# Kernel tuning notes

Hardware: AMD Instinct MI355X
Metric: run time of the kernel (lower is better)

The kernel has to match this reference:

```python
import jax, jax.numpy as jnp
import numpy as np

N_NODES = 50000
NFEAT, NHID, NSSF, NCLASS = 512, 512, 256, 64
N_EDGES = 1600000
SP_RATE = 0.5
EPS = 1e-6


def spmm(src, dst, vals, m):
    # sparse [N,N] @ dense [N,F]: gather rows by src, scale, scatter-add to dst rows
    return jax.ops.segment_sum(m[src] * vals[:, None], dst, num_segments=N_NODES)


def setup_inputs() -> dict:
    key = jax.random.key(0)
    ks = jax.random.split(key, 12)
    stdv1 = 1.0 / np.sqrt(NFEAT)
    stdv2 = 1.0 / np.sqrt(NHID)
    inp = {
        "x": jax.random.normal(ks[0], (N_NODES, NFEAT), jnp.float32),
        "src": jax.random.randint(ks[1], (N_EDGES,), 0, N_NODES, jnp.int32),
        "dst": jax.random.randint(ks[2], (N_EDGES,), 0, N_NODES, jnp.int32),
        "vals": jax.random.uniform(ks[3], (N_EDGES,), jnp.float32),
        "W1": jax.random.uniform(ks[4], (NFEAT, NHID), jnp.float32, -stdv1, stdv1),
        "b1": jax.random.uniform(ks[5], (NHID,), jnp.float32, -stdv1, stdv1),
        "W2": jax.random.uniform(ks[6], (NHID, NHID), jnp.float32, -stdv2, stdv2),
        "b2": jax.random.uniform(ks[7], (NHID,), jnp.float32, -stdv2, stdv2),
        "W3": jax.random.uniform(ks[8], (NHID, NSSF), jnp.float32, -stdv2, stdv2),
        "b3": jax.random.uniform(ks[9], (NSSF,), jnp.float32, -stdv2, stdv2),
        "ssf": jax.random.normal(ks[10], (NSSF, NCLASS), jnp.float32) * 0.1,
        "sigma": jax.random.normal(ks[11], (), jnp.float32),
    }
    return inp


def reference(x, src, dst, vals, W1, b1, W2, b2, W3, b3, ssf, sigma):
    # 3 GCN layers: spmm(adj, x @ W + b)
    h = spmm(src, dst, vals, x @ W1 + b1)
    h = jax.nn.relu(h)
    h = spmm(src, dst, vals, h @ W2 + b2)
    h = jax.nn.relu(h)
    h = spmm(src, dst, vals, h @ W3 + b3)  # [N, NSSF]

    # sparsify subspace filter by magnitude threshold (static index)
    flat = jnp.abs(ssf).reshape(-1)
    filter_idx = round(NSSF * NCLASS * SP_RATE)
    threshold = jnp.sort(flat)[filter_idx]
    ssf_sp = jnp.where(jnp.abs(ssf) >= threshold, ssf, 0.0)

    out = h @ ssf_sp  # [N, NCLASS]

    # negative euclidean distance to each filter column: cdist(h, ssf_sp.T)
    sq = (jnp.sum(h * h, axis=1)[:, None]
          - 2.0 * out
          + jnp.sum(ssf_sp * ssf_sp, axis=0)[None, :])
    spatial_dist = -jnp.sqrt(jnp.maximum(sq, 1e-12))

    # cosine similarity of each row of h with each filter column
    hn = jnp.maximum(jnp.linalg.norm(h, axis=1), EPS)          # [N]
    cn = jnp.maximum(jnp.linalg.norm(ssf_sp, axis=0), EPS)     # [NCLASS]
    spatial_similarity = out / (hn[:, None] * cn[None, :])

    spatial_loss = 0.5 * (jax.nn.log_softmax(spatial_dist, axis=1)
                          + jax.nn.log_softmax(spatial_similarity, axis=1))
    return (out, ssf_sp, h, spatial_loss, sigma)
```

## Files before the change

### kernel.cpp

```cpp
#include <hip/hip_runtime.h>
#include <hip/hip_bf16.h>
#include <cstddef>

#define NN 50000
#define NE 1600000
#define NFEAT 512
#define NHID 512
#define NSSF 256
#define NCLASS 64
#define KTH 8193

typedef unsigned short u16;
typedef unsigned int u32;
typedef u16 u16x8 __attribute__((ext_vector_type(8)));
typedef u16 u16x4 __attribute__((ext_vector_type(4)));
typedef short bf16x8 __attribute__((ext_vector_type(8)));
typedef float f32x4 __attribute__((ext_vector_type(4)));

__device__ __forceinline__ float bf2f(u16 u) {
  union { unsigned u; float f; } c; c.u = ((unsigned)u) << 16; return c.f;
}
__device__ __forceinline__ u16 f2bf(float f) {
  __hip_bfloat16 b = __float2bfloat16(f);
  union { __hip_bfloat16 b; u16 u; } c; c.b = b; return c.u;
}

__device__ __forceinline__ void async_load16(const void* g, void* l) {
  __builtin_amdgcn_global_load_lds(
      (const __attribute__((address_space(1))) unsigned int*)g,
      (__attribute__((address_space(3))) unsigned int*)l, 16, 0, 0);
}

__global__ void k_hist(const int* __restrict__ dst, int* __restrict__ cnt) {
  int i = blockIdx.x * blockDim.x + threadIdx.x;
  int stride = gridDim.x * blockDim.x;
  for (; i < NE; i += stride) atomicAdd(&cnt[dst[i]], 1);
}

#define SCAN_B 196
__global__ void k_blksum(const int* __restrict__ cnt, int* __restrict__ bsum) {
  __shared__ int red[256];
  int b = blockIdx.x, t = threadIdx.x;
  int i = b * 256 + t;
  red[t] = (i < NN) ? cnt[i] : 0;
  __syncthreads();
  for (int s = 128; s > 0; s >>= 1) { if (t < s) red[t] += red[t + s]; __syncthreads(); }
  if (t == 0) bsum[b] = red[0];
}

__global__ void k_scanb(const int* __restrict__ bsum, int* __restrict__ boff,
                        int* __restrict__ rp) {
  __shared__ int buf[256];
  int t = threadIdx.x;
  int x = (t < SCAN_B) ? bsum[t] : 0;
  buf[t] = x;
  __syncthreads();
  for (int off = 1; off < 256; off <<= 1) {
    int y = (t >= off) ? buf[t - off] : 0;
    __syncthreads();
    buf[t] += y;
    __syncthreads();
  }
  if (t < SCAN_B) boff[t] = buf[t] - x;
  if (t == 0) rp[0] = 0;
}

__global__ void k_scanf(const int* __restrict__ cnt, const int* __restrict__ boff,
                        int* __restrict__ rp, int* __restrict__ fill) {
  __shared__ int buf[256];
  int b = blockIdx.x, t = threadIdx.x;
  int i = b * 256 + t;
  int x = (i < NN) ? cnt[i] : 0;
  buf[t] = x;
  __syncthreads();
  for (int off = 1; off < 256; off <<= 1) {
    int y = (t >= off) ? buf[t - off] : 0;
    __syncthreads();
    buf[t] += y;
    __syncthreads();
  }
  if (i < NN) {
    int incl = boff[b] + buf[t];
    rp[i + 1] = incl;
    fill[i] = incl - x;
  }
}

__global__ void k_scatter(const int* __restrict__ src, const int* __restrict__ dst,
                          const float* __restrict__ vals, int* __restrict__ fill,
                          u32* __restrict__ em) {
  int i = blockIdx.x * blockDim.x + threadIdx.x;
  int stride = gridDim.x * blockDim.x;
  for (; i < NE; i += stride) {
    int p = atomicAdd(&fill[dst[i]], 1);
    em[p] = (u32)src[i] | ((u32)f2bf(vals[i]) << 16);
  }
}

__global__ void k_cvt_bf16(const float* __restrict__ x, u16* __restrict__ xb, int n4) {
  int i = blockIdx.x * blockDim.x + threadIdx.x;
  if (i < n4) {
    float4 v = *(const float4*)(x + (size_t)i * 4);
    u16x4 o;
    o[0] = f2bf(v.x); o[1] = f2bf(v.y); o[2] = f2bf(v.z); o[3] = f2bf(v.w);
    *(u16x4*)(xb + (size_t)i * 4) = o;
  }
}

__global__ void k_wt(const float* __restrict__ W, u16* __restrict__ Wt, int K, int N) {
  int idx = blockIdx.x * blockDim.x + threadIdx.x;
  if (idx < N * K) {
    int n = idx / K, k = idx % K;
    Wt[idx] = f2bf(W[(size_t)k * N + n]);
  }
}

__global__ __launch_bounds__(256, 2) void k_gemm_mfma(
    const u16* __restrict__ A, const u16* __restrict__ Bt,
    const float* __restrict__ bias, u16* __restrict__ C,
    int M, int K, int N)
{
  __shared__ __align__(16) u16 As[128 * 32];
  __shared__ __align__(16) u16 Bs[128 * 32];
  int tid = threadIdx.x;
  int bm = blockIdx.y * 128;
  int bn = blockIdx.x * 128;
  int wave = tid >> 6, lane = tid & 63;

  int lrow = lane >> 2, lcol = (lane & 3) * 8;
  int arow0 = wave * 32 + lrow;
  int arow1 = wave * 32 + 16 + lrow;
  int garow0 = bm + arow0; if (garow0 >= M) garow0 = M - 1;
  int garow1 = bm + arow1; if (garow1 >= M) garow1 = M - 1;
  const u16* Ap0 = A + (size_t)garow0 * K + lcol;
  const u16* Ap1 = A + (size_t)garow1 * K + lcol;
  const u16* Bp0 = Bt + (size_t)(bn + arow0) * K + lcol;
  const u16* Bp1 = Bt + (size_t)(bn + arow1) * K + lcol;
  u16* lA0 = &As[(wave * 32) * 32];
  u16* lA1 = &As[(wave * 32 + 16) * 32];
  u16* lB0 = &Bs[(wave * 32) * 32];
  u16* lB1 = &Bs[(wave * 32 + 16) * 32];

  int wm = (wave >> 1) * 64, wn = (wave & 1) * 64;
  int m16 = lane & 15, quad = lane >> 4;

  f32x4 zz = {0.f, 0.f, 0.f, 0.f};
  f32x4 acc[4][4];
#pragma unroll
  for (int i = 0; i < 4; i++)
#pragma unroll
    for (int j = 0; j < 4; j++) acc[i][j] = zz;

  for (int k0 = 0; k0 < K; k0 += 32) {
    async_load16(Ap0 + k0, lA0);
    async_load16(Ap1 + k0, lA1);
    async_load16(Bp0 + k0, lB0);
    async_load16(Bp1 + k0, lB1);
    __syncthreads();

    bf16x8 af[4], bw[4];
#pragma unroll
    for (int i = 0; i < 4; i++)
      af[i] = *(const bf16x8*)&As[(wm + i * 16 + m16) * 32 + quad * 8];
#pragma unroll
    for (int j = 0; j < 4; j++)
      bw[j] = *(const bf16x8*)&Bs[(wn + j * 16 + m16) * 32 + quad * 8];
#pragma unroll
    for (int i = 0; i < 4; i++)
#pragma unroll
      for (int j = 0; j < 4; j++)
        acc[i][j] = __builtin_amdgcn_mfma_f32_16x16x32_bf16(af[i], bw[j], acc[i][j], 0, 0, 0);
    __syncthreads();
  }

#pragma unroll
  for (int j = 0; j < 4; j++) {
    int col = bn + wn + j * 16 + m16;
    float bv = bias[col];
#pragma unroll
    for (int i = 0; i < 4; i++) {
      int rbase = bm + wm + i * 16 + quad * 4;
#pragma unroll
      for (int r = 0; r < 4; r++) {
        int row = rbase + r;
        if (row < M) C[(size_t)row * N + col] = f2bf(acc[i][j][r] + bv);
      }
    }
  }
}

__global__ __launch_bounds__(256) void k_spmm512(
    const int* __restrict__ rp, const u32* __restrict__ em,
    const u16* __restrict__ Xb, u16* __restrict__ Hb)
{
  int wave = threadIdx.x >> 6, lane = threadIdx.x & 63;
  int r = blockIdx.x * 4 + wave;
  if (r >= NN) return;
  int e0 = rp[r], e1 = rp[r + 1];
  float acc0[8], acc1[8];
#pragma unroll
  for (int j = 0; j < 8; j++) { acc0[j] = 0.f; acc1[j] = 0.f; }
  const u16* Xl = Xb + lane * 8;
  int e = e0;
  for (; e + 2 <= e1; e += 2) {
    u32 m0 = em[e], m1 = em[e + 1];
    float v0 = __uint_as_float(m0 & 0xFFFF0000u);
    float v1 = __uint_as_float(m1 & 0xFFFF0000u);
    u16x8 x0 = *(const u16x8*)(Xl + (size_t)(m0 & 0xFFFFu) * 512);
    u16x8 x1 = *(const u16x8*)(Xl + (size_t)(m1 & 0xFFFFu) * 512);
#pragma unroll
    for (int j = 0; j < 8; j++) {
      acc0[j] += v0 * bf2f(x0[j]);
      acc1[j] += v1 * bf2f(x1[j]);
    }
  }
  if (e < e1) {
    u32 m0 = em[e];
    float v0 = __uint_as_float(m0 & 0xFFFF0000u);
    u16x8 x0 = *(const u16x8*)(Xl + (size_t)(m0 & 0xFFFFu) * 512);
#pragma unroll
    for (int j = 0; j < 8; j++) acc0[j] += v0 * bf2f(x0[j]);
  }
  u16x8 o;
#pragma unroll
  for (int j = 0; j < 8; j++) o[j] = f2bf(fmaxf(acc0[j] + acc1[j], 0.f));
  *(u16x8*)(Hb + (size_t)r * 512 + lane * 8) = o;
}

__global__ __launch_bounds__(256) void k_spmm256(
    const int* __restrict__ rp, const u32* __restrict__ em,
    const u16* __restrict__ Xb, float* __restrict__ Hf)
{
  int wave = threadIdx.x >> 6, lane = threadIdx.x & 63;
  int r = blockIdx.x * 4 + wave;
  if (r >= NN) return;
  int e0 = rp[r], e1 = rp[r + 1];
  float4 a0 = make_float4(0.f, 0.f, 0.f, 0.f);
  float4 a1 = make_float4(0.f, 0.f, 0.f, 0.f);
  const u16* Xl = Xb + lane * 4;
  int e = e0;
  for (; e + 2 <= e1; e += 2) {
    u32 m0 = em[e], m1 = em[e + 1];
    float v0 = __uint_as_float(m0 & 0xFFFF0000u);
    float v1 = __uint_as_float(m1 & 0xFFFF0000u);
    u16x4 x0 = *(const u16x4*)(Xl + (size_t)(m0 & 0xFFFFu) * 256);
    u16x4 x1 = *(const u16x4*)(Xl + (size_t)(m1 & 0xFFFFu) * 256);
    a0.x += v0 * bf2f(x0[0]); a0.y += v0 * bf2f(x0[1]);
    a0.z += v0 * bf2f(x0[2]); a0.w += v0 * bf2f(x0[3]);
    a1.x += v1 * bf2f(x1[0]); a1.y += v1 * bf2f(x1[1]);
    a1.z += v1 * bf2f(x1[2]); a1.w += v1 * bf2f(x1[3]);
  }
  if (e < e1) {
    u32 m0 = em[e];
    float v0 = __uint_as_float(m0 & 0xFFFF0000u);
    u16x4 x0 = *(const u16x4*)(Xl + (size_t)(m0 & 0xFFFFu) * 256);
    a0.x += v0 * bf2f(x0[0]); a0.y += v0 * bf2f(x0[1]);
    a0.z += v0 * bf2f(x0[2]); a0.w += v0 * bf2f(x0[3]);
  }
  float4 o;
  o.x = a0.x + a1.x; o.y = a0.y + a1.y; o.z = a0.z + a1.z; o.w = a0.w + a1.w;
  *(float4*)(Hf + (size_t)r * 256 + lane * 4) = o;
}

__global__ void k_ssf(const float* __restrict__ ssf, const float* __restrict__ sigma,
                      float* __restrict__ o_ssf, float* __restrict__ csq,
                      float* __restrict__ cnm, float* __restrict__ o_sig)
{
  __shared__ float sv[NSSF * NCLASS];
  __shared__ int red[256];
  int tid = threadIdx.x;
  for (int i = tid; i < NSSF * NCLASS; i += 256) sv[i] = ssf[i];
  __syncthreads();
  unsigned lo = 0u, hi = 0x7f800000u;
  while (lo < hi) {
    unsigned mid = lo + ((hi - lo) >> 1);
    int c = 0;
    for (int i = tid; i < NSSF * NCLASS; i += 256)
      c += ((__float_as_uint(sv[i]) & 0x7fffffffu) <= mid) ? 1 : 0;
    red[tid] = c;
    __syncthreads();
    for (int s = 128; s > 0; s >>= 1) {
      if (tid < s) red[tid] += red[tid + s];
      __syncthreads();
    }
    int total = red[0];
    __syncthreads();
    if (total >= KTH) hi = mid; else lo = mid + 1;
  }
  float t = __uint_as_float(lo);
  for (int i = tid; i < NSSF * NCLASS; i += 256) {
    float v = sv[i];
    v = (fabsf(v) >= t) ? v : 0.f;
    sv[i] = v;
    o_ssf[i] = v;
  }
  __syncthreads();
  if (tid < 64) {
    float s = 0.f;
    for (int k = 0; k < NSSF; k++) { float v = sv[k * NCLASS + tid]; s += v * v; }
    csq[tid] = s;
    cnm[tid] = fmaxf(sqrtf(s), 1e-6f);
  }
  if (tid == 0) o_sig[0] = sigma[0];
}

__global__ __launch_bounds__(256) void k_final(
    const float* __restrict__ h, const float* __restrict__ ssf_sp,
    const float* __restrict__ colsq, const float* __restrict__ cn,
    float* __restrict__ outp, float* __restrict__ lossp)
{
  __shared__ float s_ssf[NSSF * NCLASS];
  int tid = threadIdx.x;
  for (int i = tid; i < NSSF * NCLASS; i += 256) s_ssf[i] = ssf_sp[i];
  __syncthreads();
  int wave = tid >> 6, lane = tid & 63;

  for (int r = blockIdx.x * 4 + wave; r < NN; r += gridDim.x * 4) {
    float4 hv = *(const float4*)(h + (size_t)r * NSSF + lane * 4);
    float hsq = hv.x * hv.x + hv.y * hv.y + hv.z * hv.z + hv.w * hv.w;
#pragma unroll
    for (int m = 1; m < 64; m <<= 1) hsq += __shfl_xor(hsq, m);

    float acc = 0.f;
    for (int k4 = 0; k4 < 64; ++k4) {
      float hx = __shfl(hv.x, k4);
      float hy = __shfl(hv.y, k4);
      float hz = __shfl(hv.z, k4);
      float hw = __shfl(hv.w, k4);
      const float* p = &s_ssf[k4 * 4 * NCLASS + lane];
      acc += hx * p[0] + hy * p[NCLASS] + hz * p[2 * NCLASS] + hw * p[3 * NCLASS];
    }
    float o = acc;
    outp[(size_t)r * NCLASS + lane] = o;

    float sq = hsq - 2.f * o + colsq[lane];
    float d = -sqrtf(fmaxf(sq, 1e-12f));
    float hn = fmaxf(sqrtf(hsq), 1e-6f);
    float sim = o / (hn * cn[lane]);

    float m1 = d;
#pragma unroll
    for (int m = 1; m < 64; m <<= 1) m1 = fmaxf(m1, __shfl_xor(m1, m));
    float s1 = expf(d - m1);
#pragma unroll
    for (int m = 1; m < 64; m <<= 1) s1 += __shfl_xor(s1, m);
    float ls1 = d - m1 - logf(s1);

    float m2 = sim;
#pragma unroll
    for (int m = 1; m < 64; m <<= 1) m2 = fmaxf(m2, __shfl_xor(m2, m));
    float s2 = expf(sim - m2);
#pragma unroll
    for (int m = 1; m < 64; m <<= 1) s2 += __shfl_xor(s2, m);
    float ls2 = sim - m2 - logf(s2);

    lossp[(size_t)r * NCLASS + lane] = 0.5f * (ls1 + ls2);
  }
}

extern "C" void kernel_launch(void* const* d_in, const int* in_sizes, int n_in,
                              void* d_out, int out_size, void* d_ws, size_t ws_size,
                              hipStream_t stream)
{
  (void)in_sizes; (void)n_in; (void)out_size; (void)ws_size;
  const float* x    = (const float*)d_in[0];
  const int*   src  = (const int*)  d_in[1];
  const int*   dst  = (const int*)  d_in[2];
  const float* vals = (const float*)d_in[3];
  const float* W1 = (const float*)d_in[4];
  const float* b1 = (const float*)d_in[5];
  const float* W2 = (const float*)d_in[6];
  const float* b2 = (const float*)d_in[7];
  const float* W3 = (const float*)d_in[8];
  const float* b3 = (const float*)d_in[9];
  const float* ssf   = (const float*)d_in[10];
  const float* sigma = (const float*)d_in[11];

  float* outf   = (float*)d_out;
  float* o_out  = outf;
  float* o_ssf  = outf + (size_t)NN * NCLASS;
  float* o_h    = o_ssf + NSSF * NCLASS;
  float* o_loss = o_h + (size_t)NN * NSSF;
  float* o_sig  = o_loss + (size_t)NN * NCLASS;

  u16* Xb  = (u16*)d_ws;
  u16* Yb  = Xb + (size_t)NN * NFEAT;
  u16* Hb  = Yb + (size_t)NN * NHID;
  u16* W1t = Hb + (size_t)NN * NHID;
  u16* W2t = W1t + (size_t)NFEAT * NHID;
  u16* W3t = W2t + (size_t)NHID * NHID;
  int* cnt = (int*)(W3t + (size_t)NSSF * NHID);
  int* rp  = cnt + NN;
  u32* em  = (u32*)(rp + 50016);
  int* bsum = (int*)(em + NE);
  int* boff = bsum + 256;
  float* csq = (float*)(boff + 256);
  float* cnm = csq + 64;

  hipMemsetAsync(cnt, 0, NN * sizeof(int), stream);
  k_hist<<<1024, 256, 0, stream>>>(dst, cnt);
  k_blksum<<<SCAN_B, 256, 0, stream>>>(cnt, bsum);
  k_scanb<<<1, 256, 0, stream>>>(bsum, boff, rp);
  k_scanf<<<SCAN_B, 256, 0, stream>>>(cnt, boff, rp, cnt);
  k_scatter<<<1024, 256, 0, stream>>>(src, dst, vals, cnt, em);

  k_cvt_bf16<<<(NN * NFEAT / 4 + 255) / 256, 256, 0, stream>>>(x, Xb, NN * NFEAT / 4);
  k_wt<<<(NFEAT * NHID + 255) / 256, 256, 0, stream>>>(W1, W1t, NFEAT, NHID);
  k_wt<<<(NHID * NHID + 255) / 256, 256, 0, stream>>>(W2, W2t, NHID, NHID);
  k_wt<<<(NHID * NSSF + 255) / 256, 256, 0, stream>>>(W3, W3t, NHID, NSSF);

  k_gemm_mfma<<<dim3(4, 391), 256, 0, stream>>>(Xb, W1t, b1, Yb, NN, NFEAT, NHID);
  k_spmm512<<<NN / 4, 256, 0, stream>>>(rp, em, Yb, Hb);
  k_gemm_mfma<<<dim3(4, 391), 256, 0, stream>>>(Hb, W2t, b2, Yb, NN, NHID, NHID);
  k_spmm512<<<NN / 4, 256, 0, stream>>>(rp, em, Yb, Xb);
  k_gemm_mfma<<<dim3(2, 391), 256, 0, stream>>>(Xb, W3t, b3, Yb, NN, NHID, NSSF);
  k_spmm256<<<NN / 4, 256, 0, stream>>>(rp, em, Yb, o_h);

  k_ssf<<<1, 256, 0, stream>>>(ssf, sigma, o_ssf, csq, cnm, o_sig);
  k_final<<<512, 256, 0, stream>>>(o_h, o_ssf, csq, cnm, o_out, o_loss);
}
```

Before: 1.346 ms.

## Rewrite final epilogue as bf16 MFMA GEMM with precomputed row norms

The last SpMM now also writes a bf16 copy of h and each row's squared norm. The final kernel becomes an MFMA 16x16x32 bf16 GEMM against a transposed, padded bf16 copy of the filter in shared memory, with the softmax reductions done over 16-lane groups. This replaces the scalar shuffle-and-FMA matmul and the per-row norm reduction in the epilogue. The cost is an extra bf16 write of h and lower precision for the output and loss.

```diff
diff --git a/kernel.cpp b/kernel.cpp
--- a/kernel.cpp
+++ b/kernel.cpp
@@ -229,7 +229,8 @@
 
 __global__ __launch_bounds__(256) void k_spmm256(
     const int* __restrict__ rp, const u32* __restrict__ em,
-    const u16* __restrict__ Xb, float* __restrict__ Hf)
+    const u16* __restrict__ Xb, float* __restrict__ Hf,
+    u16* __restrict__ Hb3, float* __restrict__ hsq)
 {
   int wave = threadIdx.x >> 6, lane = threadIdx.x & 63;
   int r = blockIdx.x * 4 + wave;
@@ -260,6 +261,13 @@
   float4 o;
   o.x = a0.x + a1.x; o.y = a0.y + a1.y; o.z = a0.z + a1.z; o.w = a0.w + a1.w;
   *(float4*)(Hf + (size_t)r * 256 + lane * 4) = o;
+  u16x4 ob;
+  ob[0] = f2bf(o.x); ob[1] = f2bf(o.y); ob[2] = f2bf(o.z); ob[3] = f2bf(o.w);
+  *(u16x4*)(Hb3 + (size_t)r * 256 + lane * 4) = ob;
+  float s = o.x * o.x + o.y * o.y + o.z * o.z + o.w * o.w;
+#pragma unroll
+  for (int m = 1; m < 64; m <<= 1) s += __shfl_xor(s, m);
+  if (lane == 0) hsq[r] = s;
 }
 
 __global__ void k_ssf(const float* __restrict__ ssf, const float* __restrict__ sigma,
@@ -304,57 +312,97 @@
   if (tid == 0) o_sig[0] = sigma[0];
 }
 
-__global__ __launch_bounds__(256) void k_final(
-    const float* __restrict__ h, const float* __restrict__ ssf_sp,
-    const float* __restrict__ colsq, const float* __restrict__ cn,
-    float* __restrict__ outp, float* __restrict__ lossp)
-{
-  __shared__ float s_ssf[NSSF * NCLASS];
+#define SSTR 264
+__global__ __launch_bounds__(256) void k_epi(
+    const u16* __restrict__ hb, const float* __restrict__ hsq,
+    const float* __restrict__ ssf_sp, const float* __restrict__ colsq,
+    const float* __restrict__ cn, float* __restrict__ outp,
+    float* __restrict__ lossp)
+{
+  __shared__ __align__(16) u16 sT[64 * SSTR];
   int tid = threadIdx.x;
-  for (int i = tid; i < NSSF * NCLASS; i += 256) s_ssf[i] = ssf_sp[i];
-  __syncthreads();
+  for (int i = tid; i < NCLASS * NSSF; i += 256) {
+    int n = i & 63, k = i >> 6;
+    sT[n * SSTR + k] = f2bf(ssf_sp[i]);
+  }
+  __syncthreads();
+
   int wave = tid >> 6, lane = tid & 63;
-
-  for (int r = blockIdx.x * 4 + wave; r < NN; r += gridDim.x * 4) {
-    float4 hv = *(const float4*)(h + (size_t)r * NSSF + lane * 4);
-    float hsq = hv.x * hv.x + hv.y * hv.y + hv.z * hv.z + hv.w * hv.w;
-#pragma unroll
-    for (int m = 1; m < 64; m <<= 1) hsq += __shfl_xor(hsq, m);
-
-    float acc = 0.f;
-    for (int k4 = 0; k4 < 64; ++k4) {
-      float hx = __shfl(hv.x, k4);
-      float hy = __shfl(hv.y, k4);
-      float hz = __shfl(hv.z, k4);
-      float hw = __shfl(hv.w, k4);
-      const float* p = &s_ssf[k4 * 4 * NCLASS + lane];
-      acc += hx * p[0] + hy * p[NCLASS] + hz * p[2 * NCLASS] + hw * p[3 * NCLASS];
-    }
-    float o = acc;
-    outp[(size_t)r * NCLASS + lane] = o;
-
-    float sq = hsq - 2.f * o + colsq[lane];
-    float d = -sqrtf(fmaxf(sq, 1e-12f));
-    float hn = fmaxf(sqrtf(hsq), 1e-6f);
-    float sim = o / (hn * cn[lane]);
-
-    float m1 = d;
-#pragma unroll
-    for (int m = 1; m < 64; m <<= 1) m1 = fmaxf(m1, __shfl_xor(m1, m));
-    float s1 = expf(d - m1);
-#pragma unroll
-    for (int m = 1; m < 64; m <<= 1) s1 += __shfl_xor(s1, m);
-    float ls1 = d - m1 - logf(s1);
-
-    float m2 = sim;
-#pragma unroll
-    for (int m = 1; m < 64; m <<= 1) m2 = fmaxf(m2, __shfl_xor(m2, m));
-    float s2 = expf(sim - m2);
-#pragma unroll
-    for (int m = 1; m < 64; m <<= 1) s2 += __shfl_xor(s2, m);
-    float ls2 = sim - m2 - logf(s2);
-
-    lossp[(size_t)r * NCLASS + lane] = 0.5f * (ls1 + ls2);
+  int m16 = lane & 15, quad = lane >> 4;
+  int rb = blockIdx.x * 64 + wave * 16;
+
+  int arow = rb + m16; if (arow >= NN) arow = NN - 1;
+  const u16* hp = hb + (size_t)arow * NSSF + quad * 8;
+  bf16x8 a8[8];
+#pragma unroll
+  for (int ks = 0; ks < 8; ks++) a8[ks] = *(const bf16x8*)(hp + ks * 32);
+
+  f32x4 zz = {0.f, 0.f, 0.f, 0.f};
+  f32x4 acc[4];
+#pragma unroll
+  for (int j = 0; j < 4; j++) acc[j] = zz;
+#pragma unroll
+  for (int j = 0; j < 4; j++) {
+    const u16* bp = &sT[(j * 16 + m16) * SSTR + quad * 8];
+#pragma unroll
+    for (int ks = 0; ks < 8; ks++) {
+      bf16x8 b8 = *(const bf16x8*)(bp + ks * 32);
+      acc[j] = __builtin_amdgcn_mfma_f32_16x16x32_bf16(a8[ks], b8, acc[j], 0, 0, 0);
+    }
+  }
+
+  float csql[4], cnl[4];
+#pragma unroll
+  for (int j = 0; j < 4; j++) {
+    int c = j * 16 + m16;
+    csql[j] = colsq[c];
+    cnl[j] = cn[c];
+  }
+
+#pragma unroll
+  for (int reg = 0; reg < 4; reg++) {
+    int row = rb + quad * 4 + reg;
+    bool ok = row < NN;
+    int rowc = ok ? row : NN - 1;
+    float hs = hsq[rowc];
+    float hn = fmaxf(sqrtf(hs), 1e-6f);
+    float d[4], sm[4];
+    float m1 = -3.4e38f, m2 = -3.4e38f;
+#pragma unroll
+    for (int j = 0; j < 4; j++) {
+      float o = acc[j][reg];
+      float sq = hs - 2.f * o + csql[j];
+      d[j] = -sqrtf(fmaxf(sq, 1e-12f));
+      sm[j] = o / (hn * cnl[j]);
+      m1 = fmaxf(m1, d[j]);
+      m2 = fmaxf(m2, sm[j]);
+    }
+#pragma unroll
+    for (int msk = 1; msk < 16; msk <<= 1) {
+      m1 = fmaxf(m1, __shfl_xor(m1, msk));
+      m2 = fmaxf(m2, __shfl_xor(m2, msk));
+    }
+    float s1 = 0.f, s2 = 0.f;
+#pragma unroll
+    for (int j = 0; j < 4; j++) {
+      s1 += expf(d[j] - m1);
+      s2 += expf(sm[j] - m2);
+    }
+#pragma unroll
+    for (int msk = 1; msk < 16; msk <<= 1) {
+      s1 += __shfl_xor(s1, msk);
+      s2 += __shfl_xor(s2, msk);
+    }
+    float l1 = logf(s1), l2 = logf(s2);
+    if (ok) {
+#pragma unroll
+      for (int j = 0; j < 4; j++) {
+        int c = j * 16 + m16;
+        outp[(size_t)row * NCLASS + c] = acc[j][reg];
+        lossp[(size_t)row * NCLASS + c] =
+            0.5f * ((d[j] - m1 - l1) + (sm[j] - m2 - l2));
+      }
+    }
   }
 }
 
@@ -396,6 +444,7 @@
   int* boff = bsum + 256;
   float* csq = (float*)(boff + 256);
   float* cnm = csq + 64;
+  float* hsq = cnm + 64;
 
   hipMemsetAsync(cnt, 0, NN * sizeof(int), stream);
   k_hist<<<1024, 256, 0, stream>>>(dst, cnt);
@@ -414,8 +463,8 @@
   k_gemm_mfma<<<dim3(4, 391), 256, 0, stream>>>(Hb, W2t, b2, Yb, NN, NHID, NHID);
   k_spmm512<<<NN / 4, 256, 0, stream>>>(rp, em, Yb, Xb);
   k_gemm_mfma<<<dim3(2, 391), 256, 0, stream>>>(Xb, W3t, b3, Yb, NN, NHID, NSSF);
-  k_spmm256<<<NN / 4, 256, 0, stream>>>(rp, em, Yb, o_h);
+  k_spmm256<<<NN / 4, 256, 0, stream>>>(rp, em, Yb, o_h, Hb, hsq);
 
   k_ssf<<<1, 256, 0, stream>>>(ssf, sigma, o_ssf, csq, cnm, o_sig);
-  k_final<<<512, 256, 0, stream>>>(o_h, o_ssf, csq, cnm, o_out, o_loss);
-}
+  k_epi<<<(NN + 63) / 64, 256, 0, stream>>>(Hb, hsq, o_ssf, csq, cnm, o_out, o_loss);
+}
```

Measured after the change: 1.175 ms. -12.7%, faster.
